# Optimization experiments

Hardware: AMD Instinct MI355X
Metric: run time of the kernel (lower is better)

Reference implementation:

```python
import jax, jax.numpy as jnp
import numpy as np
from jax import lax

G = 31      # grid_size
C = 16      # c (representative feature dim)
NL = 16     # n_L representative colors
CP = 128    # c_prime
S = G + 1   # corner-point spatial size = 32


def _conv(x, w, b):
    # 3x3 stride-1 pad-1 conv, NCHW / OIHW
    y = lax.conv_general_dilated(x, w, (1, 1), 'SAME',
                                 dimension_numbers=('NCHW', 'OIHW', 'NCHW'))
    return y + b[None, :, None, None]


def _bn(x, gamma, beta, mean, var):
    # eval-mode BatchNorm2d
    inv = gamma / jnp.sqrt(var + 1e-5)
    return x * inv[None, :, None, None] + (beta - mean * inv)[None, :, None, None]


def _block(x, w1, b1, g, be, m, v, w2, b2):
    # convBnSwish (stride=1) followed by plain 3x3 conv
    h = _conv(x, w1, b1)
    h = _bn(h, g, be, m, v)
    h = h * jax.nn.sigmoid(h)  # SiLU
    return _conv(h, w2, b2)


def setup_inputs() -> dict:
    key = jax.random.key(0)
    ks = jax.random.split(key, 16)
    B = 8
    d = {
        'f': jax.random.normal(ks[0], (B, C, 496, 496), jnp.float32),
        'features': jax.random.normal(ks[1], (B, CP, S, S), jnp.float32),
        # convR_L params
        'wR1': jax.random.normal(ks[2], (CP, CP, 3, 3), jnp.float32) * 0.03,
        'bR1': jnp.zeros((CP,), jnp.float32),
        'gR': jnp.ones((CP,), jnp.float32),
        'betR': jnp.zeros((CP,), jnp.float32),
        'mR': jax.random.normal(ks[3], (CP,), jnp.float32) * 0.1,
        'vR': jax.random.uniform(ks[4], (CP,), jnp.float32, 0.5, 1.5),
        'wR2': jax.random.normal(ks[5], (C * NL, CP, 3, 3), jnp.float32) * 0.03,
        'bR2': jnp.zeros((C * NL,), jnp.float32),
        # convT_L params
        'wT1': jax.random.normal(ks[6], (CP, CP, 3, 3), jnp.float32) * 0.03,
        'bT1': jnp.zeros((CP,), jnp.float32),
        'gT': jnp.ones((CP,), jnp.float32),
        'betT': jnp.zeros((CP,), jnp.float32),
        'mT': jax.random.normal(ks[7], (CP,), jnp.float32) * 0.1,
        'vT': jax.random.uniform(ks[8], (CP,), jnp.float32, 0.5, 1.5),
        'wT2': jax.random.normal(ks[9], (3 * NL, CP, 3, 3), jnp.float32) * 0.03,
        'bT2': jnp.zeros((3 * NL,), jnp.float32),
    }
    return d


def _corners(x):
    # x: [B,S,S,d,NL] -> concat 4 grid-cell corner points along color axis -> [B,G,G,d,4*NL]
    return jnp.concatenate([x[:, :-1, :-1], x[:, 1:, :-1],
                            x[:, :-1, 1:], x[:, 1:, 1:]], axis=-1)


def reference(f, features, wR1, bR1, gR, betR, mR, vR, wR2, bR2,
              wT1, bT1, gT, betT, mT, vT, wT2, bT2):
    B, _, H, W = f.shape
    hp, wp = H // G, W // G  # H,W chosen as multiples of G so padding() is a no-op

    r = _block(features, wR1, bR1, gR, betR, mR, vR, wR2, bR2)  # [B, C*NL, S, S]
    t = _block(features, wT1, bT1, gT, betT, mT, vT, wT2, bT2)  # [B, 3*NL, S, S]
    r = r.reshape(B, C, NL, S, S).transpose(0, 3, 4, 1, 2)      # [B,S,S,C,NL]
    t = t.reshape(B, 3, NL, S, S).transpose(0, 3, 4, 1, 2)      # [B,S,S,3,NL]

    r4 = _corners(r)  # [B,G,G,C,4NL]
    t4 = _corners(t)  # [B,G,G,3,4NL]

    # split f into GxG patches of (hp,wp): [B,G,G,hp*wp,C]
    fp = f.reshape(B, C, G, hp, G, wp).transpose(0, 2, 4, 3, 5, 1)
    fp = fp.reshape(B, G, G, hp * wp, C)

    scores = jnp.einsum('bijpc,bijcn->bijpn', fp, r4) / np.sqrt(C).astype(np.float32)
    att = jax.nn.softmax(scores, axis=-1)                        # [B,G,G,hp*wp,4NL]
    y = jnp.einsum('bijpn,bijdn->bijpd', att, t4)                # [B,G,G,hp*wp,3]
    y = y.reshape(B, G, G, hp, wp, 3).transpose(0, 5, 1, 3, 2, 4).reshape(B, 3, H, W)
    return y
```

## Files before the change

kernel.cpp:

```cpp
#include <hip/hip_runtime.h>
#include <hip/hip_bf16.h>
#include <stdint.h>
#include <stddef.h>

using u32 = unsigned int;
using u16 = unsigned short;

typedef short bf16x8 __attribute__((ext_vector_type(8)));
typedef _Float16 f16x8 __attribute__((ext_vector_type(8)));
typedef float f32x4 __attribute__((ext_vector_type(4)));
typedef u32  u32x4 __attribute__((ext_vector_type(4)));
typedef u32  u32x2 __attribute__((ext_vector_type(2)));

#define RSCALE 0.18033688011112042f

__device__ __forceinline__ u16 f2bf(float f) {
  u32 u = __builtin_bit_cast(u32, f);
  u32 r = (u + 0x7FFFu + ((u >> 16) & 1u)) >> 16;
  return (u16)r;
}

__device__ __forceinline__ u32 pkh(float a, float b) {
  return __builtin_bit_cast(u32, __builtin_amdgcn_cvt_pkrtz(a, b));
}

__global__ __launch_bounds__(256) void repack_kernel(
    const float* wR1, const float* wT1, const float* wR2, const float* wT2,
    const float* bR1, const float* gR, const float* betR, const float* mR, const float* vR,
    const float* bT1, const float* gT, const float* betT, const float* mT, const float* vT,
    const float* bR2, const float* bT2,
    u16* wb1, u16* wb2, float* scale1, float* shift1, float* biasC)
{
  if (blockIdx.x == 2592) {
    int t = threadIdx.x;
    float g, v, be, mm, bb;
    if (t < 128) { g = gR[t]; v = vR[t]; be = betR[t]; mm = mR[t]; bb = bR1[t]; }
    else         { g = gT[t-128]; v = vT[t-128]; be = betT[t-128]; mm = mT[t-128]; bb = bT1[t-128]; }
    float sc = g * rsqrtf(v + 1e-5f);
    scale1[t] = sc;
    shift1[t] = (bb - mm) * sc + be;
    biasC[t] = bR2[t];
    if (t < 64) biasC[256 + t] = (t < 48) ? bT2[t] : 0.0f;
    return;
  }
  int idx = blockIdx.x * 256 + threadIdx.x;
  if (idx < 294912) {
    int oc = idx / 1152, k = idx - oc * 1152;
    int tap = k >> 7, ic = k & 127;
    float w = (oc < 128) ? wR1[(oc * 128 + ic) * 9 + tap]
                         : wT1[((oc - 128) * 128 + ic) * 9 + tap];
    wb1[idx] = f2bf(w);
  } else {
    int r2 = idx - 294912;
    int oc = r2 / 1152, k = r2 - oc * 1152;
    int tap = k >> 7, ic = k & 127;
    float w;
    if (oc < 256)            w = wR2[(oc * 128 + ic) * 9 + tap];
    else if (oc - 256 < 48)  w = wT2[((oc - 256) * 128 + ic) * 9 + tap];
    else                     w = 0.0f;
    wb2[r2] = f2bf(w);
  }
}

__global__ __launch_bounds__(256) void transpose_kernel(const float* feat, u16* feat_t)
{
  __shared__ float tile[128 * 33];
  int b = blockIdx.x >> 5, y = blockIdx.x & 31;
  int t = threadIdx.x;
  const float* src = feat + (size_t)(b * 128) * 1024 + y * 32;
#pragma unroll
  for (int q = 0; q < 16; q++) {
    int idx = q * 256 + t;
    int ic = idx >> 5, x = idx & 31;
    tile[ic * 33 + x] = src[(size_t)ic * 1024 + x];
  }
  __syncthreads();
  u16* dst = feat_t + (size_t)((b * 32 + y) * 32) * 128;
#pragma unroll
  for (int q = 0; q < 16; q++) {
    int idx = q * 256 + t;
    int x = idx >> 7, ic = idx & 127;
    dst[x * 128 + ic] = f2bf(tile[ic * 33 + x]);
  }
}

template <int SRCC, int EPI>
__global__ __launch_bounds__(256) void conv_gemm_kernel(
    const u16* __restrict__ src, const u16* __restrict__ Bt,
    u16* __restrict__ out0, float* __restrict__ out1,
    const float* __restrict__ c0, const float* __restrict__ c1)
{
  __shared__ u16 As[4 * 128 * 8];
  __shared__ u16 Bs[4 * 64 * 8];
  int t = threadIdx.x;
  int lane = t & 63, wid = t >> 6;
  int wm = wid >> 1, wn = wid & 1;
  int Mbase = blockIdx.x * 128, Nbase = blockIdx.y * 64;
  int icOff = (EPI == 1 && blockIdx.y == 4) ? 128 : 0;

  int rA = t >> 2, kc = t & 3;
  int p0 = Mbase + rA, p1 = p0 + 64;
  int y0 = (p0 >> 5) & 31, x0 = p0 & 31;
  int y1 = (p1 >> 5) & 31, x1 = p1 & 31;
  const u16* aSrc0 = src + (size_t)p0 * SRCC + icOff + kc * 8;
  const u16* aSrc1 = src + (size_t)p1 * SRCC + icOff + kc * 8;
  const u16* bSrc  = Bt + (size_t)(Nbase + rA) * 1152 + kc * 8;
  u16* aDst0 = &As[kc * 1024 + rA * 8];
  u16* aDst1 = &As[kc * 1024 + (rA + 64) * 8];
  u16* bDst  = &Bs[kc * 512 + rA * 8];

  u32x4 v0, v1, vb;
  auto LOADK = [&](int kt) {
    int tap = kt >> 2;
    int dy = tap / 3 - 1, dx = tap - (tap / 3) * 3 - 1;
    int aoff = (dy * 32 + dx) * SRCC + (kt & 3) * 32;
    u32x4 z = {};
    v0 = z; v1 = z;
    if ((u32)(y0 + dy) < 32u && (u32)(x0 + dx) < 32u)
      v0 = *reinterpret_cast<const u32x4*>(aSrc0 + (ptrdiff_t)aoff);
    if ((u32)(y1 + dy) < 32u && (u32)(x1 + dx) < 32u)
      v1 = *reinterpret_cast<const u32x4*>(aSrc1 + (ptrdiff_t)aoff);
    vb = *reinterpret_cast<const u32x4*>(bSrc + kt * 32);
  };

  f32x4 acc[4][2] = {};
  LOADK(0);
  int L = lane & 15, qs = lane >> 4;
  for (int kt = 0; kt < 36; kt++) {
    __syncthreads();
    *reinterpret_cast<u32x4*>(aDst0) = v0;
    *reinterpret_cast<u32x4*>(aDst1) = v1;
    *reinterpret_cast<u32x4*>(bDst)  = vb;
    if (kt < 35) LOADK(kt + 1);
    __syncthreads();
    bf16x8 af[4], bfr2[2];
#pragma unroll
    for (int mt = 0; mt < 4; mt++)
      af[mt] = *reinterpret_cast<const bf16x8*>(&As[qs * 1024 + (wm * 64 + mt * 16 + L) * 8]);
#pragma unroll
    for (int nt = 0; nt < 2; nt++)
      bfr2[nt] = *reinterpret_cast<const bf16x8*>(&Bs[qs * 512 + (wn * 32 + nt * 16 + L) * 8]);
#pragma unroll
    for (int mt = 0; mt < 4; mt++)
#pragma unroll
      for (int nt = 0; nt < 2; nt++)
        acc[mt][nt] = __builtin_amdgcn_mfma_f32_16x16x32_bf16(af[mt], bfr2[nt], acc[mt][nt], 0, 0, 0);
  }
#pragma unroll
  for (int mt = 0; mt < 4; mt++) {
#pragma unroll
    for (int nt = 0; nt < 2; nt++) {
      int col = Nbase + wn * 32 + nt * 16 + (lane & 15);
#pragma unroll
      for (int r = 0; r < 4; r++) {
        int rowp = Mbase + wm * 64 + mt * 16 + (lane >> 4) * 4 + r;
        float v = acc[mt][nt][r];
        if (EPI == 0) {
          float yv = v * c0[col] + c1[col];
          float h = yv / (1.0f + __expf(-yv));
          out0[(size_t)rowp * 256 + col] = f2bf(h);
        } else {
          float rv = v + c0[col];
          if (col < 256) {
            reinterpret_cast<_Float16*>(out0)[(size_t)rowp * 256 + (col & 15) * 16 + (col >> 4)] =
                (_Float16)(rv * RSCALE);
          } else {
            int cT = col - 256;
            if (cT < 48) out1[(size_t)rowp * 64 + (cT & 15) * 4 + (cT >> 4)] = rv;
            else         out1[(size_t)rowp * 64 + (cT & 15) * 4 + 3] = 0.0f;
          }
        }
      }
    }
  }
}

__global__ __launch_bounds__(256) void attn_kernel(
    const float* __restrict__ f, const _Float16* __restrict__ rbuf,
    const float4* __restrict__ tbuf, float* __restrict__ out)
{
  const size_t cs = (size_t)496 * 496;
  __shared__ u16 fl[4096];
  __shared__ u16 tl[1024];
  int blk = blockIdx.x;
  int b = blk / 961, rem = blk - b * 961;
  int i = rem / 31, j = rem - i * 31;
  int t = threadIdx.x;
  int lane = t & 63, w = t >> 6;
  int q = lane >> 4, nl = lane & 15;

  {
    int a = t >> 5;
    int spy = (t >> 1) & 15;
    int half = t & 1;
    const float* fb = f + ((size_t)b * 16 + 2 * a) * cs
                        + (size_t)(i * 16 + spy) * 496 + j * 16 + half * 8;
    float4 c0a = *reinterpret_cast<const float4*>(fb);
    float4 c0b = *reinterpret_cast<const float4*>(fb + 4);
    float4 c1a = *reinterpret_cast<const float4*>(fb + cs);
    float4 c1b = *reinterpret_cast<const float4*>(fb + cs + 4);
    float lo[8] = {c0a.x, c0a.y, c0a.z, c0a.w, c0b.x, c0b.y, c0b.z, c0b.w};
    float hi[8] = {c1a.x, c1a.y, c1a.z, c1a.w, c1b.x, c1b.y, c1b.z, c1b.w};
    int base = spy * 256 + (a >> 2) * 128 + (a & 3) * 2;
#pragma unroll
    for (int p = 0; p < 8; p++) {
      int px = half * 8 + p;
      *reinterpret_cast<u32*>(&fl[base + ((px ^ spy) * 8)]) = pkh(lo[p], hi[p]);
    }
  }

  {
    int c = t & 15, lq = t >> 4;
    float v[4];
#pragma unroll
    for (int e2 = 0; e2 < 4; e2++) {
      int l4 = lq * 4 + e2;
      float vv = 0.0f;
      if (c == 3) vv = 1.0f;
      else if (c < 3) {
        int wcol = ((l4 >> 3) & 3) * 4 + (l4 & 3);
        int g = (l4 >> 5) * 2 + ((l4 >> 2) & 1);
        int ii = i + (g & 1), jj = j + (g >> 1);
        int pix = (b * 32 + ii) * 32 + jj;
        vv = reinterpret_cast<const float*>(&tbuf[(size_t)pix * 16 + wcol])[c];
      }
      v[e2] = vv;
    }
    u32x2 pp = { pkh(v[0], v[1]), pkh(v[2], v[3]) };
    *reinterpret_cast<u32x2*>(&tl[c * 64 + lq * 4]) = pp;
  }

  f16x8 bfr[4];
#pragma unroll
  for (int g = 0; g < 4; g++) {
    int ii = i + (g & 1), jj = j + (g >> 1);
    int pix = (b * 32 + ii) * 32 + jj;
    bfr[g] = *reinterpret_cast<const f16x8*>(rbuf + (size_t)pix * 256 + nl * 16 + (q & 1) * 8);
  }
  __syncthreads();

  f16x8 pb1 = *reinterpret_cast<const f16x8*>(&tl[nl * 64 + q * 8]);
  f16x8 pb2 = *reinterpret_cast<const f16x8*>(&tl[nl * 64 + 32 + q * 8]);

#pragma unroll
  for (int mt = 0; mt < 4; mt++) {
    int py = w * 4 + mt;
    f16x8 afr = *reinterpret_cast<const f16x8*>(&fl[py * 256 + (q & 1) * 128 + ((nl ^ py) & 15) * 8]);
    f32x4 z = {0.f, 0.f, 0.f, 0.f};
    f32x4 s0 = __builtin_amdgcn_mfma_f32_16x16x32_f16(bfr[0], afr, z, 0, 0, 0);
    f32x4 s1 = __builtin_amdgcn_mfma_f32_16x16x32_f16(bfr[1], afr, z, 0, 0, 0);
    f32x4 s2 = __builtin_amdgcn_mfma_f32_16x16x32_f16(bfr[2], afr, z, 0, 0, 0);
    f32x4 s3 = __builtin_amdgcn_mfma_f32_16x16x32_f16(bfr[3], afr, z, 0, 0, 0);

    float e0[4], e1[4], e2[4], e3[4];
#pragma unroll
    for (int r = 0; r < 4; r++) {
      e0[r] = exp2f(s0[r]); e1[r] = exp2f(s1[r]);
      e2[r] = exp2f(s2[r]); e3[r] = exp2f(s3[r]);
    }
    u32x4 A1u = { pkh(e0[0], e0[1]), pkh(e0[2], e0[3]),
                  pkh(e1[0], e1[1]), pkh(e1[2], e1[3]) };
    u32x4 A2u = { pkh(e2[0], e2[1]), pkh(e2[2], e2[3]),
                  pkh(e3[0], e3[1]), pkh(e3[2], e3[3]) };
    f16x8 A1 = __builtin_bit_cast(f16x8, A1u);
    f16x8 A2 = __builtin_bit_cast(f16x8, A2u);

    f32x4 d = __builtin_amdgcn_mfma_f32_16x16x32_f16(A1, pb1, z, 0, 0, 0);
    d = __builtin_amdgcn_mfma_f32_16x16x32_f16(A2, pb2, d, 0, 0, 0);

    int src = (lane & 48) | 3;
    float l0 = __shfl(d[0], src), l1 = __shfl(d[1], src),
          l2 = __shfl(d[2], src), l3 = __shfl(d[3], src);
    if (nl < 3) {
      float4 o;
      o.x = d[0] * __builtin_amdgcn_rcpf(l0);
      o.y = d[1] * __builtin_amdgcn_rcpf(l1);
      o.z = d[2] * __builtin_amdgcn_rcpf(l2);
      o.w = d[3] * __builtin_amdgcn_rcpf(l3);
      *reinterpret_cast<float4*>(out + ((size_t)b * 3 + nl) * cs
                                 + (size_t)(i * 16 + py) * 496 + j * 16 + q * 4) = o;
    }
  }
}

extern "C" void kernel_launch(void* const* d_in, const int* in_sizes, int n_in,
                              void* d_out, int out_size, void* d_ws, size_t ws_size,
                              hipStream_t stream)
{
  const float* f    = (const float*)d_in[0];
  const float* feats= (const float*)d_in[1];
  const float* wR1  = (const float*)d_in[2];
  const float* bR1  = (const float*)d_in[3];
  const float* gR   = (const float*)d_in[4];
  const float* betR = (const float*)d_in[5];
  const float* mR   = (const float*)d_in[6];
  const float* vR   = (const float*)d_in[7];
  const float* wR2  = (const float*)d_in[8];
  const float* bR2  = (const float*)d_in[9];
  const float* wT1  = (const float*)d_in[10];
  const float* bT1  = (const float*)d_in[11];
  const float* gT   = (const float*)d_in[12];
  const float* betT = (const float*)d_in[13];
  const float* mT   = (const float*)d_in[14];
  const float* vT   = (const float*)d_in[15];
  const float* wT2  = (const float*)d_in[16];
  const float* bT2  = (const float*)d_in[17];
  (void)in_sizes; (void)n_in; (void)out_size; (void)ws_size;

  char* ws = (char*)d_ws;
  u16*   wb1    = (u16*)(ws + 0);
  u16*   wb2    = (u16*)(ws + 589824);
  float* scale1 = (float*)(ws + 1327104);
  float* shift1 = scale1 + 256;
  float* biasC  = scale1 + 512;
  u16*   feat_t = (u16*)(ws + 1330432);
  u16*   hbuf   = (u16*)(ws + 3427584);
  u16*   rbuf16 = (u16*)(ws + 7621888);
  float* tbuf   = (float*)(ws + 11816192);

  repack_kernel<<<dim3(2593), dim3(256), 0, stream>>>(
      wR1, wT1, wR2, wT2, bR1, gR, betR, mR, vR, bT1, gT, betT, mT, vT,
      bR2, bT2, wb1, wb2, scale1, shift1, biasC);

  transpose_kernel<<<dim3(256), dim3(256), 0, stream>>>(feats, feat_t);

  conv_gemm_kernel<128, 0><<<dim3(64, 4), dim3(256), 0, stream>>>(
      feat_t, wb1, hbuf, nullptr, scale1, shift1);

  conv_gemm_kernel<256, 1><<<dim3(64, 5), dim3(256), 0, stream>>>(
      hbuf, wb2, rbuf16, tbuf, biasC, nullptr);

  attn_kernel<<<dim3(7688), dim3(256), 0, stream>>>(
      f, (const _Float16*)rbuf16, (const float4*)tbuf, (float*)d_out);
}
```

Measured before the change: 278.9 us.

## Process four patches per attention block with double-buffered register prefetch

```diff
diff --git a/kernel.cpp b/kernel.cpp
--- a/kernel.cpp
+++ b/kernel.cpp
@@ -180,105 +180,116 @@
     const float4* __restrict__ tbuf, float* __restrict__ out)
 {
   const size_t cs = (size_t)496 * 496;
-  __shared__ u16 fl[4096];
-  __shared__ u16 tl[1024];
+  __shared__ u16 fl[2][4096];
+  __shared__ u16 tl[2][1024];
   int blk = blockIdx.x;
-  int b = blk / 961, rem = blk - b * 961;
-  int i = rem / 31, j = rem - i * 31;
+  int b = blk / 248, rem = blk - b * 248;
+  int i = rem >> 3, jg = rem & 7;
   int t = threadIdx.x;
   int lane = t & 63, w = t >> 6;
   int q = lane >> 4, nl = lane & 15;
 
-  {
-    int a = t >> 5;
-    int spy = (t >> 1) & 15;
-    int half = t & 1;
+  int a = t >> 5, spy = (t >> 1) & 15, half = t & 1;
+  int tc = t & 15, lq = t >> 4;
+
+  float4 fr[2][4];
+  f16x8  bq[2][4];
+  float  tv[2][4];
+
+  auto LOADR = [&](int sl, int j) {
     const float* fb = f + ((size_t)b * 16 + 2 * a) * cs
                         + (size_t)(i * 16 + spy) * 496 + j * 16 + half * 8;
-    float4 c0a = *reinterpret_cast<const float4*>(fb);
-    float4 c0b = *reinterpret_cast<const float4*>(fb + 4);
-    float4 c1a = *reinterpret_cast<const float4*>(fb + cs);
-    float4 c1b = *reinterpret_cast<const float4*>(fb + cs + 4);
-    float lo[8] = {c0a.x, c0a.y, c0a.z, c0a.w, c0b.x, c0b.y, c0b.z, c0b.w};
-    float hi[8] = {c1a.x, c1a.y, c1a.z, c1a.w, c1b.x, c1b.y, c1b.z, c1b.w};
-    int base = spy * 256 + (a >> 2) * 128 + (a & 3) * 2;
-#pragma unroll
-    for (int p = 0; p < 8; p++) {
-      int px = half * 8 + p;
-      *reinterpret_cast<u32*>(&fl[base + ((px ^ spy) * 8)]) = pkh(lo[p], hi[p]);
-    }
-  }
-
-  {
-    int c = t & 15, lq = t >> 4;
-    float v[4];
+    fr[sl][0] = *reinterpret_cast<const float4*>(fb);
+    fr[sl][1] = *reinterpret_cast<const float4*>(fb + 4);
+    fr[sl][2] = *reinterpret_cast<const float4*>(fb + cs);
+    fr[sl][3] = *reinterpret_cast<const float4*>(fb + cs + 4);
+#pragma unroll
+    for (int g = 0; g < 4; g++) {
+      int ii = i + (g & 1), jj = j + (g >> 1);
+      int pix = (b * 32 + ii) * 32 + jj;
+      bq[sl][g] = *reinterpret_cast<const f16x8*>(rbuf + (size_t)pix * 256 + nl * 16 + (q & 1) * 8);
+    }
 #pragma unroll
     for (int e2 = 0; e2 < 4; e2++) {
       int l4 = lq * 4 + e2;
       float vv = 0.0f;
-      if (c == 3) vv = 1.0f;
-      else if (c < 3) {
+      if (tc == 3) vv = 1.0f;
+      else if (tc < 3) {
         int wcol = ((l4 >> 3) & 3) * 4 + (l4 & 3);
         int g = (l4 >> 5) * 2 + ((l4 >> 2) & 1);
         int ii = i + (g & 1), jj = j + (g >> 1);
         int pix = (b * 32 + ii) * 32 + jj;
-        vv = reinterpret_cast<const float*>(&tbuf[(size_t)pix * 16 + wcol])[c];
+        vv = reinterpret_cast<const float*>(&tbuf[(size_t)pix * 16 + wcol])[tc];
       }
-      v[e2] = vv;
-    }
-    u32x2 pp = { pkh(v[0], v[1]), pkh(v[2], v[3]) };
-    *reinterpret_cast<u32x2*>(&tl[c * 64 + lq * 4]) = pp;
-  }
-
-  f16x8 bfr[4];
-#pragma unroll
-  for (int g = 0; g < 4; g++) {
-    int ii = i + (g & 1), jj = j + (g >> 1);
-    int pix = (b * 32 + ii) * 32 + jj;
-    bfr[g] = *reinterpret_cast<const f16x8*>(rbuf + (size_t)pix * 256 + nl * 16 + (q & 1) * 8);
-  }
-  __syncthreads();
-
-  f16x8 pb1 = *reinterpret_cast<const f16x8*>(&tl[nl * 64 + q * 8]);
-  f16x8 pb2 = *reinterpret_cast<const f16x8*>(&tl[nl * 64 + 32 + q * 8]);
-
-#pragma unroll
-  for (int mt = 0; mt < 4; mt++) {
-    int py = w * 4 + mt;
-    f16x8 afr = *reinterpret_cast<const f16x8*>(&fl[py * 256 + (q & 1) * 128 + ((nl ^ py) & 15) * 8]);
-    f32x4 z = {0.f, 0.f, 0.f, 0.f};
-    f32x4 s0 = __builtin_amdgcn_mfma_f32_16x16x32_f16(bfr[0], afr, z, 0, 0, 0);
-    f32x4 s1 = __builtin_amdgcn_mfma_f32_16x16x32_f16(bfr[1], afr, z, 0, 0, 0);
-    f32x4 s2 = __builtin_amdgcn_mfma_f32_16x16x32_f16(bfr[2], afr, z, 0, 0, 0);
-    f32x4 s3 = __builtin_amdgcn_mfma_f32_16x16x32_f16(bfr[3], afr, z, 0, 0, 0);
-
-    float e0[4], e1[4], e2[4], e3[4];
-#pragma unroll
-    for (int r = 0; r < 4; r++) {
-      e0[r] = exp2f(s0[r]); e1[r] = exp2f(s1[r]);
-      e2[r] = exp2f(s2[r]); e3[r] = exp2f(s3[r]);
-    }
-    u32x4 A1u = { pkh(e0[0], e0[1]), pkh(e0[2], e0[3]),
-                  pkh(e1[0], e1[1]), pkh(e1[2], e1[3]) };
-    u32x4 A2u = { pkh(e2[0], e2[1]), pkh(e2[2], e2[3]),
-                  pkh(e3[0], e3[1]), pkh(e3[2], e3[3]) };
-    f16x8 A1 = __builtin_bit_cast(f16x8, A1u);
-    f16x8 A2 = __builtin_bit_cast(f16x8, A2u);
-
-    f32x4 d = __builtin_amdgcn_mfma_f32_16x16x32_f16(A1, pb1, z, 0, 0, 0);
-    d = __builtin_amdgcn_mfma_f32_16x16x32_f16(A2, pb2, d, 0, 0, 0);
-
-    int src = (lane & 48) | 3;
-    float l0 = __shfl(d[0], src), l1 = __shfl(d[1], src),
-          l2 = __shfl(d[2], src), l3 = __shfl(d[3], src);
-    if (nl < 3) {
-      float4 o;
-      o.x = d[0] * __builtin_amdgcn_rcpf(l0);
-      o.y = d[1] * __builtin_amdgcn_rcpf(l1);
-      o.z = d[2] * __builtin_amdgcn_rcpf(l2);
-      o.w = d[3] * __builtin_amdgcn_rcpf(l3);
-      *reinterpret_cast<float4*>(out + ((size_t)b * 3 + nl) * cs
-                                 + (size_t)(i * 16 + py) * 496 + j * 16 + q * 4) = o;
+      tv[sl][e2] = vv;
+    }
+  };
+
+  auto WRITELDS = [&](int sl) {
+    float4 A0 = fr[sl][0], A1 = fr[sl][1], A2 = fr[sl][2], A3 = fr[sl][3];
+    float lo[8] = {A0.x, A0.y, A0.z, A0.w, A1.x, A1.y, A1.z, A1.w};
+    float hi[8] = {A2.x, A2.y, A2.z, A2.w, A3.x, A3.y, A3.z, A3.w};
+    int base = spy * 256 + (a >> 2) * 128 + (a & 3) * 2;
+#pragma unroll
+    for (int p2 = 0; p2 < 8; p2++) {
+      int px = half * 8 + p2;
+      *reinterpret_cast<u32*>(&fl[sl][base + ((px ^ spy) * 8)]) = pkh(lo[p2], hi[p2]);
+    }
+    u32x2 pp = { pkh(tv[sl][0], tv[sl][1]), pkh(tv[sl][2], tv[sl][3]) };
+    *reinterpret_cast<u32x2*>(&tl[sl][tc * 64 + lq * 4]) = pp;
+  };
+
+  int jb = jg * 4;
+  LOADR(0, jb);
+#pragma unroll
+  for (int p = 0; p < 4; p++) {
+    int sl = p & 1;
+    int j = jb + p; if (j > 30) j = 30;
+    WRITELDS(sl);
+    if (p < 3) { int jn = jb + p + 1; if (jn > 30) jn = 30; LOADR((p + 1) & 1, jn); }
+    __syncthreads();
+
+    f16x8 pb1 = *reinterpret_cast<const f16x8*>(&tl[sl][nl * 64 + q * 8]);
+    f16x8 pb2 = *reinterpret_cast<const f16x8*>(&tl[sl][nl * 64 + 32 + q * 8]);
+#pragma unroll
+    for (int mt = 0; mt < 4; mt++) {
+      int py = w * 4 + mt;
+      f16x8 afr = *reinterpret_cast<const f16x8*>(
+          &fl[sl][py * 256 + (q & 1) * 128 + ((nl ^ py) & 15) * 8]);
+      f32x4 z = {0.f, 0.f, 0.f, 0.f};
+      f32x4 s0 = __builtin_amdgcn_mfma_f32_16x16x32_f16(bq[sl][0], afr, z, 0, 0, 0);
+      f32x4 s1 = __builtin_amdgcn_mfma_f32_16x16x32_f16(bq[sl][1], afr, z, 0, 0, 0);
+      f32x4 s2 = __builtin_amdgcn_mfma_f32_16x16x32_f16(bq[sl][2], afr, z, 0, 0, 0);
+      f32x4 s3 = __builtin_amdgcn_mfma_f32_16x16x32_f16(bq[sl][3], afr, z, 0, 0, 0);
+
+      float e0[4], e1[4], e2[4], e3[4];
+#pragma unroll
+      for (int r = 0; r < 4; r++) {
+        e0[r] = exp2f(s0[r]); e1[r] = exp2f(s1[r]);
+        e2[r] = exp2f(s2[r]); e3[r] = exp2f(s3[r]);
+      }
+      u32x4 A1u = { pkh(e0[0], e0[1]), pkh(e0[2], e0[3]),
+                    pkh(e1[0], e1[1]), pkh(e1[2], e1[3]) };
+      u32x4 A2u = { pkh(e2[0], e2[1]), pkh(e2[2], e2[3]),
+                    pkh(e3[0], e3[1]), pkh(e3[2], e3[3]) };
+      f16x8 A1 = __builtin_bit_cast(f16x8, A1u);
+      f16x8 A2 = __builtin_bit_cast(f16x8, A2u);
+
+      f32x4 d = __builtin_amdgcn_mfma_f32_16x16x32_f16(A1, pb1, z, 0, 0, 0);
+      d = __builtin_amdgcn_mfma_f32_16x16x32_f16(A2, pb2, d, 0, 0, 0);
+
+      int src = (lane & 48) | 3;
+      float l0 = __shfl(d[0], src), l1 = __shfl(d[1], src),
+            l2 = __shfl(d[2], src), l3 = __shfl(d[3], src);
+      if (nl < 3) {
+        float4 o;
+        o.x = d[0] * __builtin_amdgcn_rcpf(l0);
+        o.y = d[1] * __builtin_amdgcn_rcpf(l1);
+        o.z = d[2] * __builtin_amdgcn_rcpf(l2);
+        o.w = d[3] * __builtin_amdgcn_rcpf(l3);
+        *reinterpret_cast<float4*>(out + ((size_t)b * 3 + nl) * cs
+                                   + (size_t)(i * 16 + py) * 496 + j * 16 + q * 4) = o;
+      }
     }
   }
 }
@@ -330,6 +341,6 @@
   conv_gemm_kernel<256, 1><<<dim3(64, 5), dim3(256), 0, stream>>>(
       hbuf, wb2, rbuf16, tbuf, biasC, nullptr);
 
-  attn_kernel<<<dim3(7688), dim3(256), 0, stream>>>(
+  attn_kernel<<<dim3(1984), dim3(256), 0, stream>>>(
       f, (const _Float16*)rbuf16, (const float4*)tbuf, (float*)d_out);
 }
```

Measured after the change: 296.4 us. 1.06x slower.
